# Performance work log

Measured on AMD Instinct MI355X. Metric: run time of the kernel, lower is better.

## Reference

```python
import jax, jax.numpy as jnp
import numpy as np

VOCAB = 32000
EMBED = 1024
HIDDEN = 1024
BATCH = 256
SEQ = 1024


def setup_inputs() -> dict:
    key = jax.random.key(0)
    k1, k2, k3, k4, k5, k6 = jax.random.split(key, 6)
    x = jax.random.randint(k1, (BATCH, SEQ), 0, VOCAB)
    emb = jax.random.normal(k2, (VOCAB, EMBED), dtype=jnp.float32) * 0.02
    # nn.Linear(input_dim, hidden_dim): weight [out, in], bias [out]
    Wi = jax.random.normal(k3, (HIDDEN, EMBED), dtype=jnp.float32) * (1.0 / np.sqrt(EMBED))
    bi = jax.random.normal(k4, (HIDDEN,), dtype=jnp.float32) * 0.01
    Wh = jax.random.normal(k5, (HIDDEN, HIDDEN), dtype=jnp.float32) * (1.0 / np.sqrt(HIDDEN))
    bh = jax.random.normal(k6, (HIDDEN,), dtype=jnp.float32) * 0.01
    return {"x": x, "emb": emb, "Wi": Wi, "bi": bi, "Wh": Wh, "bh": bh}


def reference(x, emb, Wi, bi, Wh, bh):
    # Embed all tokens up front: [B, T, E]
    ex = emb[x]
    # Precompute input projection for every step (batched GEMM): [B, T, H]
    xi = jnp.einsum('bte,he->bth', ex, Wi) + bi
    h0 = jnp.zeros((x.shape[0], Wh.shape[0]), dtype=emb.dtype)

    def step(h, xi_t):  # xi_t: [B, H]
        h_new = jnp.tanh(xi_t + h @ Wh.T + bh)
        return h_new, None

    h_final, _ = jax.lax.scan(step, h0, jnp.swapaxes(xi, 0, 1))  # scan over T
    return h_final  # [B, H]
```

## Files before the change

kernel.cpp:

```cpp
#include <hip/hip_runtime.h>
#include <cmath>

#define BATCHN 256
#define SEQT   1024
#define EMBED  1024
#define HID    1024
#define VOCABN 32000

typedef __attribute__((ext_vector_type(8))) _Float16 half8;
typedef __attribute__((ext_vector_type(4))) _Float16 half4;
typedef __attribute__((ext_vector_type(4))) float    float4v;
typedef __attribute__((ext_vector_type(4))) unsigned int uint4v;
typedef __attribute__((ext_vector_type(2))) unsigned int uint2v;

#define LOSCALE 4096.0f
#define LOINV   (1.0f/4096.0f)

union FU16 { _Float16 f; unsigned short u; };
__device__ inline unsigned short f16bits(_Float16 f){ FU16 t; t.f=f; return t.u; }
__device__ inline _Float16 bits16(unsigned short u){ FU16 t; t.u=u; return t.f; }

__device__ inline void async16(const void* g, void* l) {
  __builtin_amdgcn_global_load_lds(
      (const __attribute__((address_space(1))) void*)g,
      (__attribute__((address_space(3))) void*)l, 16, 0, 0);
}

__global__ void convert_f32_f16(const float* __restrict__ in,
                                _Float16* __restrict__ out, int n) {
  int i = (blockIdx.x * blockDim.x + threadIdx.x) * 4;
  if (i + 3 < n) {
    float4v v = *reinterpret_cast<const float4v*>(in + i);
    half4 o;
#pragma unroll
    for (int j = 0; j < 4; ++j) o[j] = (_Float16)v[j];
    *reinterpret_cast<half4*>(out + i) = o;
  }
}

__global__ void split_f32_f16(const float* __restrict__ in,
                              _Float16* __restrict__ hi,
                              _Float16* __restrict__ lo, int n) {
  int i = (blockIdx.x * blockDim.x + threadIdx.x) * 4;
  if (i + 3 < n) {
    float4v v = *reinterpret_cast<const float4v*>(in + i);
    half4 h, l;
#pragma unroll
    for (int j = 0; j < 4; ++j) {
      h[j] = (_Float16)v[j];
      l[j] = (_Float16)((v[j] - (float)h[j]) * LOSCALE);
    }
    *reinterpret_cast<half4*>(hi + i) = h;
    *reinterpret_cast<half4*>(lo + i) = l;
  }
}

__global__ __launch_bounds__(256, 2) void gemm_xi(
    const _Float16* __restrict__ embh,
    const _Float16* __restrict__ Wih,
    const int* __restrict__ x,
    const float* __restrict__ bi,
    _Float16* __restrict__ xi,
    int t0, int Tc)
{
  __shared__ __align__(16) _Float16 As[128 * 64];
  __shared__ __align__(16) _Float16 Bs[128 * 64];
  __shared__ __align__(16) _Float16 stage[128 * 132];
  __shared__ int toks[128];

  const int tid  = threadIdx.x;
  const int wid  = tid >> 6, lane = tid & 63;
  const int nt   = blockIdx.x & 7, mt = blockIdx.x >> 3;
  const int m0   = mt * 128, n0 = nt * 128;

  if (tid < 128) {
    int m  = m0 + tid;
    int tl = m >> 8;
    int b  = m & 255;
    toks[tid] = x[b * SEQT + t0 + tl];
  }
  __syncthreads();

  const _Float16* aptr[4];
  const _Float16* bptr[4];
  int ldsoff[4];
#pragma unroll
  for (int i = 0; i < 4; ++i) {
    int idx = i * 256 + tid;
    int row = idx >> 3, kc = idx & 7;
    aptr[i]   = embh + (size_t)toks[row] * 1024 + kc * 8;
    bptr[i]   = Wih + ((size_t)(n0 + row) << 10) + kc * 8;
    ldsoff[i] = idx * 8;
  }

  float4v acc[4][4] = {};
  const int wm = wid & 1, wn = wid >> 1;
  const int cn = lane & 15, kg = lane >> 4;

  for (int k0 = 0; k0 < 1024; k0 += 64) {
#pragma unroll
    for (int i = 0; i < 4; ++i) {
      async16(aptr[i] + k0, &As[ldsoff[i]]);
      async16(bptr[i] + k0, &Bs[ldsoff[i]]);
    }
    __syncthreads();

    half8 a[4][2], b[4][2];
#pragma unroll
    for (int mf = 0; mf < 4; ++mf)
#pragma unroll
      for (int kf = 0; kf < 2; ++kf)
        a[mf][kf] = *reinterpret_cast<const half8*>(
            &As[(wm * 64 + mf * 16 + cn) * 64 + kf * 32 + kg * 8]);
#pragma unroll
    for (int nf = 0; nf < 4; ++nf)
#pragma unroll
      for (int kf = 0; kf < 2; ++kf)
        b[nf][kf] = *reinterpret_cast<const half8*>(
            &Bs[(wn * 64 + nf * 16 + cn) * 64 + kf * 32 + kg * 8]);

#pragma unroll
    for (int mf = 0; mf < 4; ++mf)
#pragma unroll
      for (int nf = 0; nf < 4; ++nf)
#pragma unroll
        for (int kf = 0; kf < 2; ++kf)
          acc[mf][nf] = __builtin_amdgcn_mfma_f32_16x16x32_f16(
              a[mf][kf], b[nf][kf], acc[mf][nf], 0, 0, 0);
    __syncthreads();
  }

#pragma unroll
  for (int nf = 0; nf < 4; ++nf) {
    int n = wn * 64 + nf * 16 + cn;
    float biv = bi[n0 + n];
#pragma unroll
    for (int mf = 0; mf < 4; ++mf) {
#pragma unroll
      for (int j = 0; j < 4; ++j) {
        int m = wm * 64 + mf * 16 + kg * 4 + j;
        stage[m * 132 + n] = (_Float16)(acc[mf][nf][j] + biv);
      }
    }
  }
  __syncthreads();
#pragma unroll
  for (int p = 0; p < 8; ++p) {
    int chunk = p * 256 + tid;
    int r = chunk >> 4, cc = chunk & 15;
    half4 v0 = *reinterpret_cast<const half4*>(stage + r * 132 + cc * 8);
    half4 v1 = *reinterpret_cast<const half4*>(stage + r * 132 + cc * 8 + 4);
    half8 o;
#pragma unroll
    for (int e = 0; e < 4; ++e) { o[e] = v0[e]; o[4 + e] = v1[e]; }
    int m  = m0 + r;
    int tt = m >> 8, b = m & 255;
    int n  = n0 + cc * 8;
    size_t addr = ((size_t)(tt * 256 + (b >> 4) * 16 + (n >> 6)) << 10)
                + (size_t)((b & 15) * 64 + (n & 63));
    *reinterpret_cast<half8*>(xi + addr) = o;
  }
}

__global__ __launch_bounds__(256, 1) void rnn_scan(
    const _Float16* __restrict__ Whig,
    const _Float16* __restrict__ Wlog,
    const float* __restrict__ bh,
    const _Float16* __restrict__ xi,
    float* __restrict__ hstate,
    float* __restrict__ out,
    _Float16* __restrict__ hx0, _Float16* __restrict__ lx0,
    _Float16* __restrict__ hx1, _Float16* __restrict__ lx1,
    _Float16* __restrict__ hx2, _Float16* __restrict__ lx2,
    int* __restrict__ flags,
    int t0, int Tc)
{
  __shared__ __align__(16) _Float16 Ahi[16 * 1024];
  __shared__ __align__(16) _Float16 Alo[16 * 1024];
  __shared__ __align__(16) float    part[2][4][16][68];

  const int tid  = threadIdx.x;
  const int wv   = tid >> 6, lane = tid & 63;
  const int cn   = lane & 15, kg = lane >> 4;
  const int gb   = blockIdx.x >> 4;
  const int gc   = blockIdx.x & 15;
  const int r0   = gb * 16;
  const int rowl = lane & 15;
  const int cib  = wv * 16 + ((lane >> 4) << 2);
  const int gcol = gc * 64 + cib;
  const size_t blockbase = ((size_t)(gb * 16 + gc)) << 10;

  half8 whi[32], wlo[32];
#pragma unroll
  for (int c = 0; c < 4; ++c)
#pragma unroll
    for (int kkl = 0; kkl < 8; ++kkl) {
      int col = gc * 64 + c * 16 + cn;
      int k   = (wv * 8 + kkl) * 32 + kg * 8;
      whi[c * 8 + kkl] = *reinterpret_cast<const half8*>(Whig + ((size_t)col << 10) + k);
      wlo[c * 8 + kkl] = *reinterpret_cast<const half8*>(Wlog + ((size_t)col << 10) + k);
    }
  const float4v bh4 = *reinterpret_cast<const float4v*>(bh + gcol);

  if (t0 == 0) {
#pragma unroll
    for (int p = 0; p < 8; ++p) {
      int idx = p * 256 + tid, row = idx >> 7, cc = idx & 127;
      int bo = (((row << 11) + cc * 16) ^ ((row & 7) << 4));
      half8 z = {0, 0, 0, 0, 0, 0, 0, 0};
      *reinterpret_cast<half8*>(reinterpret_cast<char*>(Ahi) + bo) = z;
      *reinterpret_cast<half8*>(reinterpret_cast<char*>(Alo) + bo) = z;
    }
  } else {
#pragma unroll
    for (int p = 0; p < 8; ++p) {
      int idx = p * 256 + tid, row = idx >> 7, cc = idx & 127;
      const float* hp = hstate + (((size_t)(r0 + row)) << 10) + cc * 8;
      half8 vh, vl;
#pragma unroll
      for (int e = 0; e < 8; ++e) {
        float f = hp[e];
        _Float16 hi = (_Float16)f;
        vh[e] = hi;
        vl[e] = (_Float16)((f - (float)hi) * LOSCALE);
      }
      int bo = (((row << 11) + cc * 16) ^ ((row & 7) << 4));
      *reinterpret_cast<half8*>(reinterpret_cast<char*>(Ahi) + bo) = vh;
      *reinterpret_cast<half8*>(reinterpret_cast<char*>(Alo) + bo) = vl;
    }
  }
  __syncthreads();

  _Float16 *cH = hx0, *cL = lx0, *nH = hx1, *nL = lx1, *oH = hx2, *oL = lx2;

  uint2v xr;
  {
    unsigned long long ap = (unsigned long long)
        (xi + blockbase + (size_t)(rowl * 64 + cib));
    asm volatile("global_load_dwordx2 %0, %1, off" : "=v"(xr) : "v"(ap) : "memory");
  }

  uint4v u1h[4], u1l[4];

#define MFMA_Q(K0, K1)                                                          \
  _Pragma("unroll")                                                             \
  for (int kkl = (K0); kkl < (K1); ++kkl) {                                     \
    int ab = (((cn << 11) + (wv * 8 + kkl) * 64 + kg * 16) ^ ((cn & 7) << 4));  \
    half8 ah = *reinterpret_cast<const half8*>(reinterpret_cast<const char*>(Ahi) + ab); \
    half8 al = *reinterpret_cast<const half8*>(reinterpret_cast<const char*>(Alo) + ab); \
    _Pragma("unroll")                                                           \
    for (int c = 0; c < 4; ++c) {                                               \
      asm("v_mfma_f32_16x16x32_f16 %0, %1, %2, %0" : "+v"(ac1[c]) : "v"(ah), "a"(whi[c * 8 + kkl])); \
      asm("v_mfma_f32_16x16x32_f16 %0, %1, %2, %0" : "+v"(ac2[c]) : "v"(al), "a"(whi[c * 8 + kkl])); \
      asm("v_mfma_f32_16x16x32_f16 %0, %1, %2, %0" : "+v"(ac3[c]) : "v"(ah), "a"(wlo[c * 8 + kkl])); \
    }                                                                           \
  }

  for (int tt = 0; tt < Tc; ++tt) {
    const int pb = tt & 1;
    float4v ac1[4] = {}, ac2[4] = {}, ac3[4] = {};

    MFMA_Q(0, 4)

    if (tt != 0) {
      asm volatile("s_waitcnt vmcnt(0)" ::: "memory");
      __builtin_amdgcn_sched_barrier(0);
#pragma unroll
      for (int p = 0; p < 4; ++p) {
        int gcbl = 2 + (p >> 1), ch = (p & 1) * 64 + lane;
        int rw = ch >> 3, c8 = ch & 7;
        int gcb = wv * 4 + gcbl;
        int bo = (((rw << 11) + gcb * 128 + c8 * 16) ^ ((rw & 7) << 4));
        *reinterpret_cast<uint4v*>(reinterpret_cast<char*>(Ahi) + bo) = u1h[p];
        *reinterpret_cast<uint4v*>(reinterpret_cast<char*>(Alo) + bo) = u1l[p];
      }
      asm volatile("s_waitcnt lgkmcnt(0)" ::: "memory");
      __builtin_amdgcn_sched_barrier(0);
    }

    MFMA_Q(4, 8)
    asm volatile("s_nop 7\n\ts_nop 7");

#pragma unroll
    for (int c = 0; c < 4; ++c)
#pragma unroll
      for (int j = 0; j < 4; ++j)
        part[pb][wv][kg * 4 + j][c * 16 + cn] =
            ac1[c][j] + (ac2[c][j] + ac3[c][j]) * LOINV;
    __syncthreads();

    float4v vs = {};
#pragma unroll
    for (int w = 0; w < 4; ++w) {
      float4v pw = *reinterpret_cast<const float4v*>(&part[pb][w][rowl][cib]);
#pragma unroll
      for (int j = 0; j < 4; ++j) vs[j] += pw[j];
    }
    asm volatile("s_waitcnt vmcnt(0)" ::: "memory");

    const int tglob = t0 + tt;
    float hv[4];
    unsigned short hu[4], lu[4];
#pragma unroll
    for (int cj = 0; cj < 4; ++cj) {
      unsigned int w = (cj < 2) ? xr[0] : xr[1];
      unsigned short xb = (cj & 1) ? (unsigned short)(w >> 16) : (unsigned short)(w & 0xffffu);
      float v = vs[cj] + bh4[cj] + (float)bits16(xb);
      float ex = __expf(2.0f * v);
      float h  = 1.0f - 2.0f / (ex + 1.0f);
      hv[cj] = h;
      FU16 thi, tlo;
      thi.f = (_Float16)h;
      tlo.f = (_Float16)((h - (float)thi.f) * LOSCALE);
      hu[cj] = thi.u; lu[cj] = tlo.u;
    }
    if (tt < Tc - 1) {
      uint2v ph, pl;
      ph[0] = (unsigned int)hu[0] | ((unsigned int)hu[1] << 16);
      ph[1] = (unsigned int)hu[2] | ((unsigned int)hu[3] << 16);
      pl[0] = (unsigned int)lu[0] | ((unsigned int)lu[1] << 16);
      pl[1] = (unsigned int)lu[2] | ((unsigned int)lu[3] << 16);
      size_t off = blockbase + (size_t)(rowl * 64 + cib);
      asm volatile("global_store_dwordx2 %0, %1, off sc0 sc1"
                   :: "v"((unsigned long long)(cH + off)), "v"(ph) : "memory");
      asm volatile("global_store_dwordx2 %0, %1, off sc0 sc1"
                   :: "v"((unsigned long long)(cL + off)), "v"(pl) : "memory");
    }
    if (tglob == SEQT - 1) {
      float4v o = {hv[0], hv[1], hv[2], hv[3]};
      *reinterpret_cast<float4v*>(out + (((size_t)(r0 + rowl)) << 10) + gcol) = o;
    } else if (tt == Tc - 1) {
      float4v o = {hv[0], hv[1], hv[2], hv[3]};
      *reinterpret_cast<float4v*>(hstate + (((size_t)(r0 + rowl)) << 10) + gcol) = o;
    }
    if (tt == Tc - 1) break;

    asm volatile("s_waitcnt vmcnt(0)" ::: "memory");
    const int target = tt + 1;
    if (lane == 0)
      asm volatile("global_store_dword %0, %1, off sc0 sc1"
                   :: "v"((unsigned long long)(flags + ((gb * 16 + gc) * 4 + wv) * 32)),
                      "v"(target) : "memory");

    {
      unsigned long long ap = (unsigned long long)
          (xi + blockbase + (((size_t)(tt + 1)) << 18) + (size_t)(rowl * 64 + cib));
      asm volatile("global_load_dwordx2 %0, %1, off" : "=v"(xr) : "v"(ap) : "memory");
    }

    if (lane < 16) {
      int pgc = wv * 4 + (lane >> 2), pwv = lane & 3;
      const int* fp = flags + ((gb * 16 + pgc) * 4 + pwv) * 32;
      for (;;) {
        int v;
        asm volatile("global_load_dword %0, %1, off sc0 sc1\n\t"
                     "s_waitcnt vmcnt(0)"
                     : "=v"(v) : "v"((unsigned long long)fp) : "memory");
        if (v >= target) break;
        __builtin_amdgcn_s_sleep(1);
      }
    }

    uint4v u0h[4], u0l[4];
#pragma unroll
    for (int p = 0; p < 4; ++p) {
      int gcbl = p >> 1, ch = (p & 1) * 64 + lane;
      int rw = ch >> 3, c8 = ch & 7;
      int gcb = wv * 4 + gcbl;
      size_t off = (((size_t)(gb * 16 + gcb)) << 10) + rw * 64 + c8 * 8;
      asm volatile("global_load_dwordx4 %0, %1, off sc0 sc1"
                   : "=v"(u0h[p]) : "v"((unsigned long long)(cH + off)) : "memory");
      asm volatile("global_load_dwordx4 %0, %1, off sc0 sc1"
                   : "=v"(u0l[p]) : "v"((unsigned long long)(cL + off)) : "memory");
    }
#pragma unroll
    for (int p = 0; p < 4; ++p) {
      int gcbl = 2 + (p >> 1), ch = (p & 1) * 64 + lane;
      int rw = ch >> 3, c8 = ch & 7;
      int gcb = wv * 4 + gcbl;
      size_t off = (((size_t)(gb * 16 + gcb)) << 10) + rw * 64 + c8 * 8;
      asm volatile("global_load_dwordx4 %0, %1, off sc0 sc1"
                   : "=v"(u1h[p]) : "v"((unsigned long long)(cH + off)) : "memory");
      asm volatile("global_load_dwordx4 %0, %1, off sc0 sc1"
                   : "=v"(u1l[p]) : "v"((unsigned long long)(cL + off)) : "memory");
    }
    asm volatile("s_waitcnt vmcnt(8)" ::: "memory");
    __builtin_amdgcn_sched_barrier(0);
#pragma unroll
    for (int p = 0; p < 4; ++p) {
      int gcbl = p >> 1, ch = (p & 1) * 64 + lane;
      int rw = ch >> 3, c8 = ch & 7;
      int gcb = wv * 4 + gcbl;
      int bo = (((rw << 11) + gcb * 128 + c8 * 16) ^ ((rw & 7) << 4));
      *reinterpret_cast<uint4v*>(reinterpret_cast<char*>(Ahi) + bo) = u0h[p];
      *reinterpret_cast<uint4v*>(reinterpret_cast<char*>(Alo) + bo) = u0l[p];
    }
    asm volatile("s_waitcnt lgkmcnt(0)" ::: "memory");
    __builtin_amdgcn_sched_barrier(0);

    _Float16* th = cH; cH = nH; nH = oH; oH = th;
    _Float16* tl = cL; cL = nL; nL = oL; oL = tl;
  }
#undef MFMA_Q
}

extern "C" void kernel_launch(void* const* d_in, const int* in_sizes, int n_in,
                              void* d_out, int out_size, void* d_ws, size_t ws_size,
                              hipStream_t stream) {
  const int*   x   = (const int*)  d_in[0];
  const float* emb = (const float*)d_in[1];
  const float* Wi  = (const float*)d_in[2];
  const float* bi  = (const float*)d_in[3];
  const float* Wh  = (const float*)d_in[4];
  const float* bh  = (const float*)d_in[5];
  float* out = (float*)d_out;

  char* ws = (char*)d_ws;
  size_t off = 0;
  auto alloc = [&](size_t bytes) -> void* {
    void* p = ws + off;
    off = (off + bytes + 255) & ~(size_t)255;
    return p;
  };

  _Float16* embh   = (_Float16*)alloc((size_t)VOCABN * EMBED * 2);
  _Float16* Wih    = (_Float16*)alloc((size_t)HID * EMBED * 2);
  _Float16* Whih   = (_Float16*)alloc((size_t)HID * HID * 2);
  _Float16* Wloh   = (_Float16*)alloc((size_t)HID * HID * 2);
  float*    hstate = (float*)   alloc((size_t)BATCHN * HID * 4);
  _Float16* hx0 = (_Float16*)alloc((size_t)BATCHN * HID * 2);
  _Float16* lx0 = (_Float16*)alloc((size_t)BATCHN * HID * 2);
  _Float16* hx1 = (_Float16*)alloc((size_t)BATCHN * HID * 2);
  _Float16* lx1 = (_Float16*)alloc((size_t)BATCHN * HID * 2);
  _Float16* hx2 = (_Float16*)alloc((size_t)BATCHN * HID * 2);
  _Float16* lx2 = (_Float16*)alloc((size_t)BATCHN * HID * 2);
  int* flags = (int*)alloc(16 * 16 * 4 * 32 * 4);
  size_t fixed = off;

  int Tc = 1024;
  while (Tc > 4 && fixed + (size_t)BATCHN * Tc * HID * 2 > ws_size) Tc >>= 1;
  _Float16* xih = (_Float16*)alloc((size_t)BATCHN * Tc * HID * 2);

  {
    int n = VOCABN * EMBED;
    convert_f32_f16<<<n / 1024, 256, 0, stream>>>(emb, embh, n);
    n = HID * EMBED;
    convert_f32_f16<<<n / 1024, 256, 0, stream>>>(Wi, Wih, n);
    n = HID * HID;
    split_f32_f16<<<n / 1024, 256, 0, stream>>>(Wh, Whih, Wloh, n);
  }

  for (int t0 = 0; t0 < SEQT; t0 += Tc) {
    int grid = (BATCHN * Tc / 128) * 8;
    gemm_xi<<<grid, 256, 0, stream>>>(embh, Wih, x, bi, xih, t0, Tc);
    hipMemsetAsync(flags, 0, 16 * 16 * 4 * 32 * 4, stream);
    rnn_scan<<<256, 256, 0, stream>>>(Whih, Wloh, bh, xih, hstate, out,
                                      hx0, lx0, hx1, lx1, hx2, lx2, flags, t0, Tc);
  }
}
```

Before: 5.704 ms.

## Aggregate per-wave step flags into one per-block flag via LDS counter

Each wave now bumps a shared-memory counter after its global stores complete. Only the last wave of a block publishes a single per-block ready flag, so each wave polls 4 flags instead of 16. The hidden-state exchange buffers go from three to two, alternating by step parity, and the step-end __syncthreads becomes an explicit lgkmcnt wait plus s_barrier. The goal is lower inter-block synchronization latency on each recurrent step. The cost is a serial LDS atomic on the critical path and more delicate cross-wave memory ordering.

```diff
diff --git a/kernel.cpp b/kernel.cpp
--- a/kernel.cpp
+++ b/kernel.cpp
@@ -169,15 +169,17 @@
     const _Float16* __restrict__ xi,
     float* __restrict__ hstate,
     float* __restrict__ out,
-    _Float16* __restrict__ hx0, _Float16* __restrict__ lx0,
-    _Float16* __restrict__ hx1, _Float16* __restrict__ lx1,
-    _Float16* __restrict__ hx2, _Float16* __restrict__ lx2,
-    int* __restrict__ flags,
+    _Float16* __restrict__ hexHiA,
+    _Float16* __restrict__ hexLoA,
+    _Float16* __restrict__ hexHiB,
+    _Float16* __restrict__ hexLoB,
+    int* __restrict__ bar,
     int t0, int Tc)
 {
   __shared__ __align__(16) _Float16 Ahi[16 * 1024];
   __shared__ __align__(16) _Float16 Alo[16 * 1024];
   __shared__ __align__(16) float    part[2][4][16][68];
+  __shared__ int wcnt;
 
   const int tid  = threadIdx.x;
   const int wv   = tid >> 6, lane = tid & 63;
@@ -202,6 +204,8 @@
     }
   const float4v bh4 = *reinterpret_cast<const float4v*>(bh + gcol);
 
+  if (tid == 0) wcnt = 0;
+
   if (t0 == 0) {
 #pragma unroll
     for (int p = 0; p < 8; ++p) {
@@ -230,8 +234,6 @@
     }
   }
   __syncthreads();
-
-  _Float16 *cH = hx0, *cL = lx0, *nH = hx1, *nL = lx1, *oH = hx2, *oL = lx2;
 
   uint2v xr;
   {
@@ -287,7 +289,9 @@
       for (int j = 0; j < 4; ++j)
         part[pb][wv][kg * 4 + j][c * 16 + cn] =
             ac1[c][j] + (ac2[c][j] + ac3[c][j]) * LOINV;
-    __syncthreads();
+    asm volatile("s_waitcnt lgkmcnt(0)" ::: "memory");
+    __builtin_amdgcn_sched_barrier(0);
+    __builtin_amdgcn_s_barrier();
 
     float4v vs = {};
 #pragma unroll
@@ -299,6 +303,9 @@
     asm volatile("s_waitcnt vmcnt(0)" ::: "memory");
 
     const int tglob = t0 + tt;
+    const int par = (tt + 1) & 1;
+    _Float16* WHi = par ? hexHiA : hexHiB;
+    _Float16* WLo = par ? hexLoA : hexLoB;
     float hv[4];
     unsigned short hu[4], lu[4];
 #pragma unroll
@@ -322,9 +329,9 @@
       pl[1] = (unsigned int)lu[2] | ((unsigned int)lu[3] << 16);
       size_t off = blockbase + (size_t)(rowl * 64 + cib);
       asm volatile("global_store_dwordx2 %0, %1, off sc0 sc1"
-                   :: "v"((unsigned long long)(cH + off)), "v"(ph) : "memory");
+                   :: "v"((unsigned long long)(WHi + off)), "v"(ph) : "memory");
       asm volatile("global_store_dwordx2 %0, %1, off sc0 sc1"
-                   :: "v"((unsigned long long)(cL + off)), "v"(pl) : "memory");
+                   :: "v"((unsigned long long)(WLo + off)), "v"(pl) : "memory");
     }
     if (tglob == SEQT - 1) {
       float4v o = {hv[0], hv[1], hv[2], hv[3]};
@@ -337,10 +344,14 @@
 
     asm volatile("s_waitcnt vmcnt(0)" ::: "memory");
     const int target = tt + 1;
-    if (lane == 0)
-      asm volatile("global_store_dword %0, %1, off sc0 sc1"
-                   :: "v"((unsigned long long)(flags + ((gb * 16 + gc) * 4 + wv) * 32)),
-                      "v"(target) : "memory");
+    if (lane == 0) {
+      int old = __hip_atomic_fetch_add(&wcnt, 1, __ATOMIC_RELAXED,
+                                       __HIP_MEMORY_SCOPE_WORKGROUP);
+      if (old == 4 * tt + 3)
+        asm volatile("global_store_dword %0, %1, off sc0 sc1"
+                     :: "v"((unsigned long long)(bar + (gb * 16 + gc) * 32)),
+                        "v"(target) : "memory");
+    }
 
     {
       unsigned long long ap = (unsigned long long)
@@ -348,9 +359,8 @@
       asm volatile("global_load_dwordx2 %0, %1, off" : "=v"(xr) : "v"(ap) : "memory");
     }
 
-    if (lane < 16) {
-      int pgc = wv * 4 + (lane >> 2), pwv = lane & 3;
-      const int* fp = flags + ((gb * 16 + pgc) * 4 + pwv) * 32;
+    if (lane < 4) {
+      const int* fp = bar + (gb * 16 + wv * 4 + lane) * 32;
       for (;;) {
         int v;
         asm volatile("global_load_dword %0, %1, off sc0 sc1\n\t"
@@ -361,6 +371,8 @@
       }
     }
 
+    const _Float16* SHi = par ? hexHiA : hexHiB;
+    const _Float16* SLo = par ? hexLoA : hexLoB;
     uint4v u0h[4], u0l[4];
 #pragma unroll
     for (int p = 0; p < 4; ++p) {
@@ -369,9 +381,9 @@
       int gcb = wv * 4 + gcbl;
       size_t off = (((size_t)(gb * 16 + gcb)) << 10) + rw * 64 + c8 * 8;
       asm volatile("global_load_dwordx4 %0, %1, off sc0 sc1"
-                   : "=v"(u0h[p]) : "v"((unsigned long long)(cH + off)) : "memory");
+                   : "=v"(u0h[p]) : "v"((unsigned long long)(SHi + off)) : "memory");
       asm volatile("global_load_dwordx4 %0, %1, off sc0 sc1"
-                   : "=v"(u0l[p]) : "v"((unsigned long long)(cL + off)) : "memory");
+                   : "=v"(u0l[p]) : "v"((unsigned long long)(SLo + off)) : "memory");
     }
 #pragma unroll
     for (int p = 0; p < 4; ++p) {
@@ -380,9 +392,9 @@
       int gcb = wv * 4 + gcbl;
       size_t off = (((size_t)(gb * 16 + gcb)) << 10) + rw * 64 + c8 * 8;
       asm volatile("global_load_dwordx4 %0, %1, off sc0 sc1"
-                   : "=v"(u1h[p]) : "v"((unsigned long long)(cH + off)) : "memory");
+                   : "=v"(u1h[p]) : "v"((unsigned long long)(SHi + off)) : "memory");
       asm volatile("global_load_dwordx4 %0, %1, off sc0 sc1"
-                   : "=v"(u1l[p]) : "v"((unsigned long long)(cL + off)) : "memory");
+                   : "=v"(u1l[p]) : "v"((unsigned long long)(SLo + off)) : "memory");
     }
     asm volatile("s_waitcnt vmcnt(8)" ::: "memory");
     __builtin_amdgcn_sched_barrier(0);
@@ -397,9 +409,6 @@
     }
     asm volatile("s_waitcnt lgkmcnt(0)" ::: "memory");
     __builtin_amdgcn_sched_barrier(0);
-
-    _Float16* th = cH; cH = nH; nH = oH; oH = th;
-    _Float16* tl = cL; cL = nL; nL = oL; oL = tl;
   }
 #undef MFMA_Q
 }
@@ -428,13 +437,11 @@
   _Float16* Whih   = (_Float16*)alloc((size_t)HID * HID * 2);
   _Float16* Wloh   = (_Float16*)alloc((size_t)HID * HID * 2);
   float*    hstate = (float*)   alloc((size_t)BATCHN * HID * 4);
-  _Float16* hx0 = (_Float16*)alloc((size_t)BATCHN * HID * 2);
-  _Float16* lx0 = (_Float16*)alloc((size_t)BATCHN * HID * 2);
-  _Float16* hx1 = (_Float16*)alloc((size_t)BATCHN * HID * 2);
-  _Float16* lx1 = (_Float16*)alloc((size_t)BATCHN * HID * 2);
-  _Float16* hx2 = (_Float16*)alloc((size_t)BATCHN * HID * 2);
-  _Float16* lx2 = (_Float16*)alloc((size_t)BATCHN * HID * 2);
-  int* flags = (int*)alloc(16 * 16 * 4 * 32 * 4);
+  _Float16* hexHiA = (_Float16*)alloc((size_t)BATCHN * HID * 2);
+  _Float16* hexLoA = (_Float16*)alloc((size_t)BATCHN * HID * 2);
+  _Float16* hexHiB = (_Float16*)alloc((size_t)BATCHN * HID * 2);
+  _Float16* hexLoB = (_Float16*)alloc((size_t)BATCHN * HID * 2);
+  int* bar  = (int*)alloc(256 * 32 * 4);
   size_t fixed = off;
 
   int Tc = 1024;
@@ -453,8 +460,8 @@
   for (int t0 = 0; t0 < SEQT; t0 += Tc) {
     int grid = (BATCHN * Tc / 128) * 8;
     gemm_xi<<<grid, 256, 0, stream>>>(embh, Wih, x, bi, xih, t0, Tc);
-    hipMemsetAsync(flags, 0, 16 * 16 * 4 * 32 * 4, stream);
+    hipMemsetAsync(bar, 0, 256 * 32 * 4, stream);
     rnn_scan<<<256, 256, 0, stream>>>(Whih, Wloh, bh, xih, hstate, out,
-                                      hx0, lx0, hx1, lx1, hx2, lx2, flags, t0, Tc);
-  }
-}
+                                      hexHiA, hexLoA, hexHiB, hexLoB, bar, t0, Tc);
+  }
+}
```

After: 5.283 ms. 7.4% less time.
